# Kernel tuning notes

Hardware: AMD Instinct MI355X
Metric: run time of the kernel (lower is better)

The kernel has to match this reference:

```python
import jax, jax.numpy as jnp
import numpy as np

VOCAB, H, E, B, S = 50257, 1024, 1024, 64, 2048


def setup_inputs() -> dict:
    key = jax.random.key(0)
    ks = jax.random.split(key, 12)
    s = 0.02
    return {
        "input_seq": jax.random.randint(ks[0], (B,), 0, VOCAB),
        "last_hidden": jax.random.normal(ks[1], (1, B, H), jnp.float32),
        "last_cell": jax.random.normal(ks[2], (1, B, H), jnp.float32),
        "encoder_outputs": jax.random.normal(ks[3], (S, B, H), jnp.float32),
        "emb_W": jax.random.normal(ks[4], (VOCAB, E), jnp.float32) * s,
        "W_ih": jax.random.normal(ks[5], (4 * H, E), jnp.float32) * s,
        "W_hh": jax.random.normal(ks[6], (4 * H, H), jnp.float32) * s,
        "b_ih": jnp.zeros((4 * H,), jnp.float32),
        "b_hh": jnp.zeros((4 * H,), jnp.float32),
        "concat_W": jax.random.normal(ks[7], (H, 2 * H), jnp.float32) * s,
        "concat_b": jnp.zeros((H,), jnp.float32),
        "out_W": jax.random.normal(ks[8], (VOCAB, H), jnp.float32) * s,
        "out_b": jnp.zeros((VOCAB,), jnp.float32),
    }


def reference(input_seq, last_hidden, last_cell, encoder_outputs,
              emb_W, W_ih, W_hh, b_ih, b_hh,
              concat_W, concat_b, out_W, out_b):
    # Embedding lookup (dropout is identity in eval mode)
    x = emb_W[input_seq]                      # [B, E]
    h0 = last_hidden[0]                       # [B, H]
    c0 = last_cell[0]                         # [B, H]
    # Single LSTM step (PyTorch gate order: i, f, g, o)
    gates = x @ W_ih.T + b_ih + h0 @ W_hh.T + b_hh   # [B, 4H]
    i, f, g, o = jnp.split(gates, 4, axis=-1)
    c = jax.nn.sigmoid(f) * c0 + jax.nn.sigmoid(i) * jnp.tanh(g)
    h = jax.nn.sigmoid(o) * jnp.tanh(c)       # [B, H] == rnn_output
    # 'dot' attention: energies[b, s] = h[b] . enc[s, b]  (vectorized)
    energies = jnp.einsum('bh,sbh->bs', h, encoder_outputs)   # [B, S]
    attn = jax.nn.softmax(energies, axis=1)                   # [B, S]
    context = jnp.einsum('bs,sbh->bh', attn, encoder_outputs) # [B, H]
    concat_out = jnp.tanh(jnp.concatenate([h, context], axis=1) @ concat_W.T + concat_b)
    output = concat_out @ out_W.T + out_b                     # [B, VOCAB]
    return output, h[None], c[None], attn[:, None, :]
```

## Files before the change

### kernel.cpp

```cpp
#include <hip/hip_runtime.h>
#include <hip/hip_bf16.h>
#include <math.h>

#define BB 64
#define HH 1024
#define SS 2048
#define VV 50257

typedef float f32x4 __attribute__((ext_vector_type(4)));
typedef short bf16x8 __attribute__((ext_vector_type(8)));

__device__ __forceinline__ float sigf(float x){ return 1.0f/(1.0f+__expf(-x)); }
__device__ __forceinline__ short f2bf(float f){
  __hip_bfloat16 h = __float2bfloat16(f);
  return __builtin_bit_cast(short, h);
}

__global__ void k_embed(const int* __restrict__ seq, const float* __restrict__ embW,
                        float* __restrict__ x){
  int b = blockIdx.x;
  int k = threadIdx.x * 4;
  const float4 v = *reinterpret_cast<const float4*>(embW + (size_t)seq[b]*HH + k);
  *reinterpret_cast<float4*>(x + (size_t)b*HH + k) = v;
}

__global__ __launch_bounds__(256)
void k_gemm(const float* __restrict__ A1, const float* __restrict__ W1,
            const float* __restrict__ A2, const float* __restrict__ W2,
            float* __restrict__ dst, int N, int K, int ldw)
{
  __shared__ float As[64][33];
  __shared__ float Ws[128][33];
  const int tid = threadIdx.x;
  const int nb = blockIdx.x, sk = blockIdx.y, SK = gridDim.y;
  const int ntiles = 2 * (K >> 5);
  const int tps = ntiles / SK;
  const int t0 = sk * tps;
  const int bg = tid & 15, ng = tid >> 4;

  float acc[4][8];
  #pragma unroll
  for (int i = 0; i < 4; ++i)
    #pragma unroll
    for (int j = 0; j < 8; ++j) acc[i][j] = 0.f;

  const int ar = tid >> 2, ac = (tid & 3) * 8;
  const int wr = tid >> 1, wc = (tid & 1) * 16;
  const int wn = nb * 128 + wr;

  for (int t = t0; t < t0 + tps; ++t) {
    const int kt = t << 5;
    const float* A; const float* W; int kk;
    if (kt < K) { A = A1; W = W1; kk = kt; } else { A = A2; W = W2; kk = kt - K; }
    {
      const float* s = A + (size_t)ar * K + kk + ac;
      float4 v0 = *(const float4*)s;
      float4 v1 = *(const float4*)(s + 4);
      As[ar][ac+0]=v0.x; As[ar][ac+1]=v0.y; As[ar][ac+2]=v0.z; As[ar][ac+3]=v0.w;
      As[ar][ac+4]=v1.x; As[ar][ac+5]=v1.y; As[ar][ac+6]=v1.z; As[ar][ac+7]=v1.w;
    }
    if (wn < N) {
      const float* s = W + (size_t)wn * ldw + kk + wc;
      float4 v0 = *(const float4*)s;
      float4 v1 = *(const float4*)(s + 4);
      float4 v2 = *(const float4*)(s + 8);
      float4 v3 = *(const float4*)(s + 12);
      Ws[wr][wc+0]=v0.x;  Ws[wr][wc+1]=v0.y;  Ws[wr][wc+2]=v0.z;  Ws[wr][wc+3]=v0.w;
      Ws[wr][wc+4]=v1.x;  Ws[wr][wc+5]=v1.y;  Ws[wr][wc+6]=v1.z;  Ws[wr][wc+7]=v1.w;
      Ws[wr][wc+8]=v2.x;  Ws[wr][wc+9]=v2.y;  Ws[wr][wc+10]=v2.z; Ws[wr][wc+11]=v2.w;
      Ws[wr][wc+12]=v3.x; Ws[wr][wc+13]=v3.y; Ws[wr][wc+14]=v3.z; Ws[wr][wc+15]=v3.w;
    }
    __syncthreads();
    #pragma unroll 8
    for (int k = 0; k < 32; ++k) {
      const float a0 = As[bg*4+0][k], a1 = As[bg*4+1][k];
      const float a2 = As[bg*4+2][k], a3 = As[bg*4+3][k];
      #pragma unroll
      for (int j = 0; j < 8; ++j) {
        const float w = Ws[ng*8+j][k];
        acc[0][j] += a0*w; acc[1][j] += a1*w; acc[2][j] += a2*w; acc[3][j] += a3*w;
      }
    }
    __syncthreads();
  }

  #pragma unroll
  for (int j = 0; j < 8; ++j) {
    const int n = nb*128 + ng*8 + j;
    if (n < N)
      #pragma unroll
      for (int i = 0; i < 4; ++i)
        dst[((size_t)sk*64 + (bg*4+i))*N + n] = acc[i][j];
  }
}

__global__ __launch_bounds__(256)
void k_mfma(const short* __restrict__ A, int lda,
            const float* __restrict__ W1, const float* __restrict__ W2,
            int K1, int ldw, const float* __restrict__ bias,
            float* __restrict__ dst, short* __restrict__ dstb,
            int N, int Ktot, int direct, int act)
{
  const int tid  = threadIdx.x;
  const int wave = tid >> 6, lane = tid & 63;
  const int nb = blockIdx.x, sk = blockIdx.y, SK = gridDim.y;
  const int ksteps = Ktot >> 5;
  const int kps = ksteps / SK;
  const int k0 = sk * kps;
  const int n0 = nb*128 + wave*32;
  const int r = lane & 15, g = lane >> 4;

  f32x4 acc[4][2] = {};

  for (int ks = k0; ks < k0 + kps; ++ks) {
    const int kk = (ks << 5) + g*8;
    bf16x8 af[4];
    #pragma unroll
    for (int mf = 0; mf < 4; ++mf)
      af[mf] = *(const bf16x8*)(A + (size_t)(mf*16 + r)*lda + kk);
    #pragma unroll
    for (int nf = 0; nf < 2; ++nf) {
      const int n = n0 + nf*16 + r;
      bf16x8 bfr = {};
      if (n < N) {
        const float* wp = (kk < K1) ? (W1 + (size_t)n*ldw + kk)
                                    : (W2 + (size_t)n*ldw + (kk - K1));
        float4 w0 = *(const float4*)wp;
        float4 w1 = *(const float4*)(wp + 4);
        bfr[0]=f2bf(w0.x); bfr[1]=f2bf(w0.y); bfr[2]=f2bf(w0.z); bfr[3]=f2bf(w0.w);
        bfr[4]=f2bf(w1.x); bfr[5]=f2bf(w1.y); bfr[6]=f2bf(w1.z); bfr[7]=f2bf(w1.w);
      }
      #pragma unroll
      for (int mf = 0; mf < 4; ++mf)
        acc[mf][nf] = __builtin_amdgcn_mfma_f32_16x16x32_bf16(af[mf], bfr, acc[mf][nf], 0, 0, 0);
    }
  }

  if (direct) {
    #pragma unroll
    for (int nf = 0; nf < 2; ++nf) {
      const int n = n0 + nf*16 + r;
      if (n < N) {
        const float bv = bias ? bias[n] : 0.f;
        #pragma unroll
        for (int mf = 0; mf < 4; ++mf)
          #pragma unroll
          for (int j = 0; j < 4; ++j) {
            float v = acc[mf][nf][j] + bv;
            if (act == 1) v = tanhf(v);
            const int row = mf*16 + g*4 + j;
            if (dst)  dst[(size_t)row*N + n] = v;
            if (dstb) dstb[(size_t)row*N + n] = f2bf(v);
          }
      }
    }
  } else {
    #pragma unroll
    for (int nf = 0; nf < 2; ++nf) {
      const int n = n0 + nf*16 + r;
      if (n < N)
        #pragma unroll
        for (int mf = 0; mf < 4; ++mf)
          #pragma unroll
          for (int j = 0; j < 4; ++j)
            dst[((size_t)sk*64 + (mf*16 + g*4 + j))*N + n] = acc[mf][nf][j];
    }
  }
}

__global__ void k_reduce(const float* __restrict__ part, const float* __restrict__ bias1,
                         const float* __restrict__ bias2, float* __restrict__ dst,
                         short* __restrict__ dstb, int N, int SK, int act){
  size_t idx = (size_t)blockIdx.x*256 + threadIdx.x;
  if (idx >= (size_t)64*N) return;
  int b = (int)(idx / N), n = (int)(idx % N);
  float v = (bias1 ? bias1[n] : 0.f) + (bias2 ? bias2[n] : 0.f);
  for (int s = 0; s < SK; ++s) v += part[((size_t)s*64 + b)*N + n];
  if (act == 1) v = tanhf(v);
  if (dst)  dst[(size_t)b*N + n] = v;
  if (dstb) dstb[(size_t)b*N + n] = f2bf(v);
}

__global__ void k_lstm(const float* __restrict__ gates, const float* __restrict__ c0,
                       float* __restrict__ h_out, float* __restrict__ c_out,
                       short* __restrict__ concA){
  int idx = blockIdx.x*256 + threadIdx.x;
  int b = idx >> 10, k = idx & 1023;
  const float* g = gates + (size_t)b*4096;
  float gi = g[k], gf = g[1024+k], gg = g[2048+k], go = g[3072+k];
  float c = sigf(gf)*c0[idx] + sigf(gi)*tanhf(gg);
  float h = sigf(go)*tanhf(c);
  c_out[idx] = c;
  h_out[idx] = h;
  concA[(size_t)b*2048 + k] = f2bf(h);
}

__global__ __launch_bounds__(256)
void k_attn_part(const float* __restrict__ h, const float* __restrict__ enc,
                 float* __restrict__ energ, float* __restrict__ mpart,
                 float* __restrict__ lpart, float* __restrict__ ctxpart, int C){
  const int b  = blockIdx.x & 63;
  const int ch = blockIdx.x >> 6;
  const int wave = threadIdx.x >> 6;
  const int lane = threadIdx.x & 63;
  const int rows = SS / C;
  const int s0 = ch * rows;

  float4 hv0, hv1, hv2, hv3;
  {
    const float* hb = h + (size_t)b*HH + lane*16;
    hv0 = *(const float4*)(hb);   hv1 = *(const float4*)(hb+4);
    hv2 = *(const float4*)(hb+8); hv3 = *(const float4*)(hb+12);
  }
  float m = -INFINITY, l = 0.f;
  float cacc[16];
  #pragma unroll
  for (int j = 0; j < 16; ++j) cacc[j] = 0.f;

  for (int s = s0 + wave; s < s0 + rows; s += 4) {
    const float* ep = enc + ((size_t)s*BB + b)*HH + lane*16;
    const float4 e0 = *(const float4*)(ep);
    const float4 e1 = *(const float4*)(ep+4);
    const float4 e2 = *(const float4*)(ep+8);
    const float4 e3 = *(const float4*)(ep+12);
    float p = hv0.x*e0.x + hv0.y*e0.y + hv0.z*e0.z + hv0.w*e0.w
            + hv1.x*e1.x + hv1.y*e1.y + hv1.z*e1.z + hv1.w*e1.w
            + hv2.x*e2.x + hv2.y*e2.y + hv2.z*e2.z + hv2.w*e2.w
            + hv3.x*e3.x + hv3.y*e3.y + hv3.z*e3.z + hv3.w*e3.w;
    p += __shfl_xor(p, 1);  p += __shfl_xor(p, 2);  p += __shfl_xor(p, 4);
    p += __shfl_xor(p, 8);  p += __shfl_xor(p, 16); p += __shfl_xor(p, 32);
    if (lane == 0) energ[(size_t)b*SS + s] = p;
    const float mn = fmaxf(m, p);
    const float sc = __expf(m - mn);
    const float pe = __expf(p - mn);
    l = l*sc + pe;
    cacc[0]=cacc[0]*sc+pe*e0.x;  cacc[1]=cacc[1]*sc+pe*e0.y;
    cacc[2]=cacc[2]*sc+pe*e0.z;  cacc[3]=cacc[3]*sc+pe*e0.w;
    cacc[4]=cacc[4]*sc+pe*e1.x;  cacc[5]=cacc[5]*sc+pe*e1.y;
    cacc[6]=cacc[6]*sc+pe*e1.z;  cacc[7]=cacc[7]*sc+pe*e1.w;
    cacc[8]=cacc[8]*sc+pe*e2.x;  cacc[9]=cacc[9]*sc+pe*e2.y;
    cacc[10]=cacc[10]*sc+pe*e2.z; cacc[11]=cacc[11]*sc+pe*e2.w;
    cacc[12]=cacc[12]*sc+pe*e3.x; cacc[13]=cacc[13]*sc+pe*e3.y;
    cacc[14]=cacc[14]*sc+pe*e3.z; cacc[15]=cacc[15]*sc+pe*e3.w;
    m = mn;
  }

  __shared__ float sm[4], sl[4];
  __shared__ float sctx[4][1024];
  if (lane == 0) { sm[wave] = m; sl[wave] = l; }
  __syncthreads();
  const float mg = fmaxf(fmaxf(sm[0], sm[1]), fmaxf(sm[2], sm[3]));
  const float lg = sl[0]*__expf(sm[0]-mg) + sl[1]*__expf(sm[1]-mg)
                 + sl[2]*__expf(sm[2]-mg) + sl[3]*__expf(sm[3]-mg);
  const float scw = __expf(m - mg);
  #pragma unroll
  for (int j = 0; j < 16; ++j) sctx[wave][lane*16 + j] = cacc[j]*scw;
  __syncthreads();
  const int d = threadIdx.x * 4;
  const float4 a0 = *(const float4*)&sctx[0][d];
  const float4 a1 = *(const float4*)&sctx[1][d];
  const float4 a2 = *(const float4*)&sctx[2][d];
  const float4 a3 = *(const float4*)&sctx[3][d];
  float4 rr;
  rr.x = a0.x+a1.x+a2.x+a3.x; rr.y = a0.y+a1.y+a2.y+a3.y;
  rr.z = a0.z+a1.z+a2.z+a3.z; rr.w = a0.w+a1.w+a2.w+a3.w;
  *(float4*)(ctxpart + ((size_t)(b*C + ch))*HH + d) = rr;
  if (threadIdx.x == 0) { mpart[b*C+ch] = mg; lpart[b*C+ch] = lg; }
}

__global__ void k_attn_fin(const float* __restrict__ mpart, const float* __restrict__ lpart,
                           const float* __restrict__ ctxpart, const float* __restrict__ energ,
                           float* __restrict__ ctx, float* __restrict__ attn,
                           short* __restrict__ concA, int C){
  const int b = blockIdx.x, tid = threadIdx.x;
  float m = -INFINITY;
  for (int c = 0; c < C; ++c) m = fmaxf(m, mpart[b*C+c]);
  float l = 0.f;
  for (int c = 0; c < C; ++c) l += lpart[b*C+c] * __expf(mpart[b*C+c] - m);
  const float inv = 1.0f / l;
  float ax = 0.f, ay = 0.f, az = 0.f, aw = 0.f;
  for (int c = 0; c < C; ++c) {
    const float w = __expf(mpart[b*C+c] - m);
    const float* cp = ctxpart + ((size_t)(b*C+c))*HH + tid*4;
    ax += w*cp[0]; ay += w*cp[1]; az += w*cp[2]; aw += w*cp[3];
  }
  ax *= inv; ay *= inv; az *= inv; aw *= inv;
  float* o = ctx + (size_t)b*HH + tid*4;
  o[0] = ax; o[1] = ay; o[2] = az; o[3] = aw;
  short* ca = concA + (size_t)b*2048 + 1024 + tid*4;
  ca[0] = f2bf(ax); ca[1] = f2bf(ay); ca[2] = f2bf(az); ca[3] = f2bf(aw);
  for (int j = 0; j < 8; ++j) {
    const int s = j*256 + tid;
    attn[(size_t)b*SS + s] = __expf(energ[(size_t)b*SS + s] - m) * inv;
  }
}

extern "C" void kernel_launch(void* const* d_in, const int* in_sizes, int n_in,
                              void* d_out, int out_size, void* d_ws, size_t ws_size,
                              hipStream_t stream){
  const int*   seq  = (const int*)  d_in[0];
  const float* h0   = (const float*)d_in[1];
  const float* c0   = (const float*)d_in[2];
  const float* enc  = (const float*)d_in[3];
  const float* embW = (const float*)d_in[4];
  const float* W_ih = (const float*)d_in[5];
  const float* W_hh = (const float*)d_in[6];
  const float* b_ih = (const float*)d_in[7];
  const float* b_hh = (const float*)d_in[8];
  const float* cW   = (const float*)d_in[9];
  const float* cb   = (const float*)d_in[10];
  const float* oW   = (const float*)d_in[11];
  const float* ob   = (const float*)d_in[12];
  float* out = (float*)d_out;

  float* ws = (float*)d_ws;
  const size_t o_x = 0, o_gates = 65536, o_energ = 327680, o_ctx = 458752,
               o_concA = 524288, o_concB = 589824, o_dyn = 622592;
  const size_t SKPART = 4194304;
  int C = 32;
  for (;;) {
    size_t need = (o_dyn + (size_t)C*128 + (size_t)C*65536 + SKPART) * sizeof(float);
    if (need <= ws_size || C == 1) break;
    C >>= 1;
  }
  float* x       = ws + o_x;
  float* gates   = ws + o_gates;
  float* energ   = ws + o_energ;
  float* ctx     = ws + o_ctx;
  short* concA   = (short*)(ws + o_concA);
  short* concB   = (short*)(ws + o_concB);
  float* mpart   = ws + o_dyn;
  float* lpart   = mpart + (size_t)64*C;
  float* ctxpart = lpart + (size_t)64*C;
  float* skpart  = ctxpart + (size_t)64*C*1024;

  const size_t o_h = 3216448, o_c = 3281984, o_attn = 3347520;

  k_embed<<<64, 256, 0, stream>>>(seq, embW, x);

  k_gemm<<<dim3(32,16), 256, 0, stream>>>(x, W_ih, h0, W_hh, skpart, 4096, 1024, 1024);
  k_reduce<<<1024, 256, 0, stream>>>(skpart, b_ih, b_hh, gates, nullptr, 4096, 16, 0);

  k_lstm<<<256, 256, 0, stream>>>(gates, c0, out + o_h, out + o_c, concA);

  k_attn_part<<<64*C, 256, 0, stream>>>(out + o_h, enc, energ, mpart, lpart, ctxpart, C);
  k_attn_fin<<<64, 256, 0, stream>>>(mpart, lpart, ctxpart, energ, ctx,
                                     out + o_attn, concA, C);

  k_mfma<<<dim3(8,32), 256, 0, stream>>>(concA, 2048, cW, nullptr, 2048, 2048,
                                         nullptr, skpart, nullptr, 1024, 2048, 0, 0);
  k_reduce<<<256, 256, 0, stream>>>(skpart, cb, nullptr, nullptr, concB, 1024, 32, 1);

  k_mfma<<<dim3(393,1), 256, 0, stream>>>(concB, 1024, oW, nullptr, 1024, 1024,
                                          ob, out, nullptr, 50257, 1024, 1, 0);
}
```

Before: 271.6 us.

## Fuse embedding gather, bias-reduce and LSTM; pipeline logits GEMM loads

Folds the embedding gather into the gates GEMM by indexing emb_W rows directly. It merges the split-K reduction with the LSTM cell update, so two launches and the gates round trip disappear. A dedicated logits kernel software-pipelines its fp32 weight loads one k-step ahead, and the attention partial kernel processes two sequence rows per iteration. It also halves the split-K factor for the concat GEMM and drops the unused ctx store. The pipelined logits kernel uses more registers, and the smaller split-K reduces parallelism for the concat GEMM.

```diff
diff --git a/kernel.cpp b/kernel.cpp
--- a/kernel.cpp
+++ b/kernel.cpp
@@ -16,25 +16,17 @@
   return __builtin_bit_cast(short, h);
 }
 
-__global__ void k_embed(const int* __restrict__ seq, const float* __restrict__ embW,
-                        float* __restrict__ x){
-  int b = blockIdx.x;
-  int k = threadIdx.x * 4;
-  const float4 v = *reinterpret_cast<const float4*>(embW + (size_t)seq[b]*HH + k);
-  *reinterpret_cast<float4*>(x + (size_t)b*HH + k) = v;
-}
-
 __global__ __launch_bounds__(256)
-void k_gemm(const float* __restrict__ A1, const float* __restrict__ W1,
-            const float* __restrict__ A2, const float* __restrict__ W2,
-            float* __restrict__ dst, int N, int K, int ldw)
+void k_gates(const int* __restrict__ seq, const float* __restrict__ embW,
+             const float* __restrict__ h0,
+             const float* __restrict__ W_ih, const float* __restrict__ W_hh,
+             float* __restrict__ dst)
 {
   __shared__ float As[64][33];
   __shared__ float Ws[128][33];
   const int tid = threadIdx.x;
   const int nb = blockIdx.x, sk = blockIdx.y, SK = gridDim.y;
-  const int ntiles = 2 * (K >> 5);
-  const int tps = ntiles / SK;
+  const int tps = 64 / SK;
   const int t0 = sk * tps;
   const int bg = tid & 15, ng = tid >> 4;
 
@@ -47,20 +39,27 @@
   const int ar = tid >> 2, ac = (tid & 3) * 8;
   const int wr = tid >> 1, wc = (tid & 1) * 16;
   const int wn = nb * 128 + wr;
+  const int erow = seq[ar];
 
   for (int t = t0; t < t0 + tps; ++t) {
     const int kt = t << 5;
-    const float* A; const float* W; int kk;
-    if (kt < K) { A = A1; W = W1; kk = kt; } else { A = A2; W = W2; kk = kt - K; }
+    const float* abase; const float* wbase;
+    if (kt < 1024) {
+      abase = embW + (size_t)erow*1024 + kt;
+      wbase = W_ih + (size_t)wn*1024 + kt;
+    } else {
+      abase = h0 + (size_t)ar*1024 + (kt - 1024);
+      wbase = W_hh + (size_t)wn*1024 + (kt - 1024);
+    }
     {
-      const float* s = A + (size_t)ar * K + kk + ac;
+      const float* s = abase + ac;
       float4 v0 = *(const float4*)s;
       float4 v1 = *(const float4*)(s + 4);
       As[ar][ac+0]=v0.x; As[ar][ac+1]=v0.y; As[ar][ac+2]=v0.z; As[ar][ac+3]=v0.w;
       As[ar][ac+4]=v1.x; As[ar][ac+5]=v1.y; As[ar][ac+6]=v1.z; As[ar][ac+7]=v1.w;
     }
-    if (wn < N) {
-      const float* s = W + (size_t)wn * ldw + kk + wc;
+    {
+      const float* s = wbase + wc;
       float4 v0 = *(const float4*)s;
       float4 v1 = *(const float4*)(s + 4);
       float4 v2 = *(const float4*)(s + 8);
@@ -87,19 +86,38 @@
   #pragma unroll
   for (int j = 0; j < 8; ++j) {
     const int n = nb*128 + ng*8 + j;
-    if (n < N)
-      #pragma unroll
-      for (int i = 0; i < 4; ++i)
-        dst[((size_t)sk*64 + (bg*4+i))*N + n] = acc[i][j];
-  }
+    #pragma unroll
+    for (int i = 0; i < 4; ++i)
+      dst[((size_t)sk*64 + (bg*4+i))*4096 + n] = acc[i][j];
+  }
+}
+
+__global__ void k_rlstm(const float* __restrict__ part, const float* __restrict__ b_ih,
+                        const float* __restrict__ b_hh, const float* __restrict__ c0,
+                        float* __restrict__ h_out, float* __restrict__ c_out,
+                        short* __restrict__ concA, int SK){
+  int idx = blockIdx.x*256 + threadIdx.x;
+  int b = idx >> 10, k = idx & 1023;
+  float gi = b_ih[k]      + b_hh[k];
+  float gf = b_ih[1024+k] + b_hh[1024+k];
+  float gg = b_ih[2048+k] + b_hh[2048+k];
+  float go = b_ih[3072+k] + b_hh[3072+k];
+  const float* p = part + (size_t)b*4096 + k;
+  for (int s = 0; s < SK; ++s) {
+    const float* ps = p + (size_t)s*64*4096;
+    gi += ps[0]; gf += ps[1024]; gg += ps[2048]; go += ps[3072];
+  }
+  float c = sigf(gf)*c0[idx] + sigf(gi)*tanhf(gg);
+  float h = sigf(go)*tanhf(c);
+  c_out[idx] = c;
+  h_out[idx] = h;
+  concA[(size_t)b*2048 + k] = f2bf(h);
 }
 
 __global__ __launch_bounds__(256)
 void k_mfma(const short* __restrict__ A, int lda,
-            const float* __restrict__ W1, const float* __restrict__ W2,
-            int K1, int ldw, const float* __restrict__ bias,
-            float* __restrict__ dst, short* __restrict__ dstb,
-            int N, int Ktot, int direct, int act)
+            const float* __restrict__ W1, int ldw,
+            float* __restrict__ dst, int N, int Ktot)
 {
   const int tid  = threadIdx.x;
   const int wave = tid >> 6, lane = tid & 63;
@@ -121,78 +139,105 @@
     #pragma unroll
     for (int nf = 0; nf < 2; ++nf) {
       const int n = n0 + nf*16 + r;
-      bf16x8 bfr = {};
-      if (n < N) {
-        const float* wp = (kk < K1) ? (W1 + (size_t)n*ldw + kk)
-                                    : (W2 + (size_t)n*ldw + (kk - K1));
-        float4 w0 = *(const float4*)wp;
-        float4 w1 = *(const float4*)(wp + 4);
-        bfr[0]=f2bf(w0.x); bfr[1]=f2bf(w0.y); bfr[2]=f2bf(w0.z); bfr[3]=f2bf(w0.w);
-        bfr[4]=f2bf(w1.x); bfr[5]=f2bf(w1.y); bfr[6]=f2bf(w1.z); bfr[7]=f2bf(w1.w);
-      }
+      const float* wp = W1 + (size_t)n*ldw + kk;
+      float4 w0 = *(const float4*)wp;
+      float4 w1 = *(const float4*)(wp + 4);
+      bf16x8 bfr;
+      bfr[0]=f2bf(w0.x); bfr[1]=f2bf(w0.y); bfr[2]=f2bf(w0.z); bfr[3]=f2bf(w0.w);
+      bfr[4]=f2bf(w1.x); bfr[5]=f2bf(w1.y); bfr[6]=f2bf(w1.z); bfr[7]=f2bf(w1.w);
       #pragma unroll
       for (int mf = 0; mf < 4; ++mf)
         acc[mf][nf] = __builtin_amdgcn_mfma_f32_16x16x32_bf16(af[mf], bfr, acc[mf][nf], 0, 0, 0);
     }
   }
 
-  if (direct) {
+  #pragma unroll
+  for (int nf = 0; nf < 2; ++nf) {
+    const int n = n0 + nf*16 + r;
     #pragma unroll
-    for (int nf = 0; nf < 2; ++nf) {
-      const int n = n0 + nf*16 + r;
-      if (n < N) {
-        const float bv = bias ? bias[n] : 0.f;
-        #pragma unroll
-        for (int mf = 0; mf < 4; ++mf)
-          #pragma unroll
-          for (int j = 0; j < 4; ++j) {
-            float v = acc[mf][nf][j] + bv;
-            if (act == 1) v = tanhf(v);
-            const int row = mf*16 + g*4 + j;
-            if (dst)  dst[(size_t)row*N + n] = v;
-            if (dstb) dstb[(size_t)row*N + n] = f2bf(v);
-          }
-      }
-    }
-  } else {
-    #pragma unroll
-    for (int nf = 0; nf < 2; ++nf) {
-      const int n = n0 + nf*16 + r;
-      if (n < N)
-        #pragma unroll
-        for (int mf = 0; mf < 4; ++mf)
-          #pragma unroll
-          for (int j = 0; j < 4; ++j)
-            dst[((size_t)sk*64 + (mf*16 + g*4 + j))*N + n] = acc[mf][nf][j];
-    }
-  }
-}
-
-__global__ void k_reduce(const float* __restrict__ part, const float* __restrict__ bias1,
-                         const float* __restrict__ bias2, float* __restrict__ dst,
-                         short* __restrict__ dstb, int N, int SK, int act){
+    for (int mf = 0; mf < 4; ++mf)
+      #pragma unroll
+      for (int j = 0; j < 4; ++j)
+        dst[((size_t)sk*64 + (mf*16 + g*4 + j))*N + n] = acc[mf][nf][j];
+  }
+}
+
+__global__ void k_reduce(const float* __restrict__ part, const float* __restrict__ bias,
+                         short* __restrict__ dstb, int N, int SK){
   size_t idx = (size_t)blockIdx.x*256 + threadIdx.x;
   if (idx >= (size_t)64*N) return;
   int b = (int)(idx / N), n = (int)(idx % N);
-  float v = (bias1 ? bias1[n] : 0.f) + (bias2 ? bias2[n] : 0.f);
+  float v = bias[n];
   for (int s = 0; s < SK; ++s) v += part[((size_t)s*64 + b)*N + n];
-  if (act == 1) v = tanhf(v);
-  if (dst)  dst[(size_t)b*N + n] = v;
-  if (dstb) dstb[(size_t)b*N + n] = f2bf(v);
-}
-
-__global__ void k_lstm(const float* __restrict__ gates, const float* __restrict__ c0,
-                       float* __restrict__ h_out, float* __restrict__ c_out,
-                       short* __restrict__ concA){
-  int idx = blockIdx.x*256 + threadIdx.x;
-  int b = idx >> 10, k = idx & 1023;
-  const float* g = gates + (size_t)b*4096;
-  float gi = g[k], gf = g[1024+k], gg = g[2048+k], go = g[3072+k];
-  float c = sigf(gf)*c0[idx] + sigf(gi)*tanhf(gg);
-  float h = sigf(go)*tanhf(c);
-  c_out[idx] = c;
-  h_out[idx] = h;
-  concA[(size_t)b*2048 + k] = f2bf(h);
+  dstb[(size_t)b*N + n] = f2bf(tanhf(v));
+}
+
+__global__ __launch_bounds__(256)
+void k_logits(const short* __restrict__ A, const float* __restrict__ W,
+              const float* __restrict__ bias, float* __restrict__ out)
+{
+  const int tid = threadIdx.x;
+  const int wave = tid >> 6, lane = tid & 63;
+  const int r = lane & 15, g = lane >> 4;
+  const int n0 = blockIdx.x*128 + wave*32;
+  const int nA = n0 + r, nB = n0 + 16 + r;
+  const float* wA = W + (size_t)(nA < VV ? nA : 0)*1024;
+  const float* wB = W + (size_t)(nB < VV ? nB : 0)*1024;
+  const short* A0 = A + (size_t)r*1024 + g*8;
+
+  f32x4 acc[4][2] = {};
+
+  bf16x8 a0,a1,a2,a3; float4 u0,u1,v0,v1;
+  {
+    const int kk = g*8;
+    a0 = *(const bf16x8*)(A0);
+    a1 = *(const bf16x8*)(A0 + 16*1024);
+    a2 = *(const bf16x8*)(A0 + 32*1024);
+    a3 = *(const bf16x8*)(A0 + 48*1024);
+    u0 = *(const float4*)(wA + kk); u1 = *(const float4*)(wA + kk + 4);
+    v0 = *(const float4*)(wB + kk); v1 = *(const float4*)(wB + kk + 4);
+  }
+
+  #pragma unroll
+  for (int ks = 0; ks < 32; ++ks) {
+    bf16x8 ca0=a0, ca1=a1, ca2=a2, ca3=a3;
+    float4 cu0=u0, cu1=u1, cv0=v0, cv1=v1;
+    if (ks < 31) {
+      const int kk = (ks+1)*32 + g*8;
+      a0 = *(const bf16x8*)(A0 + (ks+1)*32);
+      a1 = *(const bf16x8*)(A0 + 16*1024 + (ks+1)*32);
+      a2 = *(const bf16x8*)(A0 + 32*1024 + (ks+1)*32);
+      a3 = *(const bf16x8*)(A0 + 48*1024 + (ks+1)*32);
+      u0 = *(const float4*)(wA + kk); u1 = *(const float4*)(wA + kk + 4);
+      v0 = *(const float4*)(wB + kk); v1 = *(const float4*)(wB + kk + 4);
+    }
+    bf16x8 bA, bB;
+    bA[0]=f2bf(cu0.x); bA[1]=f2bf(cu0.y); bA[2]=f2bf(cu0.z); bA[3]=f2bf(cu0.w);
+    bA[4]=f2bf(cu1.x); bA[5]=f2bf(cu1.y); bA[6]=f2bf(cu1.z); bA[7]=f2bf(cu1.w);
+    bB[0]=f2bf(cv0.x); bB[1]=f2bf(cv0.y); bB[2]=f2bf(cv0.z); bB[3]=f2bf(cv0.w);
+    bB[4]=f2bf(cv1.x); bB[5]=f2bf(cv1.y); bB[6]=f2bf(cv1.z); bB[7]=f2bf(cv1.w);
+    acc[0][0] = __builtin_amdgcn_mfma_f32_16x16x32_bf16(ca0, bA, acc[0][0], 0,0,0);
+    acc[1][0] = __builtin_amdgcn_mfma_f32_16x16x32_bf16(ca1, bA, acc[1][0], 0,0,0);
+    acc[2][0] = __builtin_amdgcn_mfma_f32_16x16x32_bf16(ca2, bA, acc[2][0], 0,0,0);
+    acc[3][0] = __builtin_amdgcn_mfma_f32_16x16x32_bf16(ca3, bA, acc[3][0], 0,0,0);
+    acc[0][1] = __builtin_amdgcn_mfma_f32_16x16x32_bf16(ca0, bB, acc[0][1], 0,0,0);
+    acc[1][1] = __builtin_amdgcn_mfma_f32_16x16x32_bf16(ca1, bB, acc[1][1], 0,0,0);
+    acc[2][1] = __builtin_amdgcn_mfma_f32_16x16x32_bf16(ca2, bB, acc[2][1], 0,0,0);
+    acc[3][1] = __builtin_amdgcn_mfma_f32_16x16x32_bf16(ca3, bB, acc[3][1], 0,0,0);
+  }
+
+  #pragma unroll
+  for (int nf = 0; nf < 2; ++nf) {
+    const int n = n0 + nf*16 + r;
+    if (n < VV) {
+      const float bv = bias[n];
+      #pragma unroll
+      for (int mf = 0; mf < 4; ++mf)
+        #pragma unroll
+        for (int j = 0; j < 4; ++j)
+          out[(size_t)(mf*16 + g*4 + j)*VV + n] = acc[mf][nf][j] + bv;
+    }
+  }
 }
 
 __global__ __launch_bounds__(256)
@@ -204,7 +249,8 @@
   const int wave = threadIdx.x >> 6;
   const int lane = threadIdx.x & 63;
   const int rows = SS / C;
-  const int s0 = ch * rows;
+  const int rpw  = rows >> 2;
+  const int sw = ch*rows + wave*rpw;
 
   float4 hv0, hv1, hv2, hv3;
   {
@@ -217,31 +263,56 @@
   #pragma unroll
   for (int j = 0; j < 16; ++j) cacc[j] = 0.f;
 
-  for (int s = s0 + wave; s < s0 + rows; s += 4) {
-    const float* ep = enc + ((size_t)s*BB + b)*HH + lane*16;
+  for (int i = 0; i < rpw; i += 2) {
+    const float* ep = enc + ((size_t)(sw+i)*BB + b)*HH + lane*16;
+    const float* fp = ep + (size_t)BB*HH;
     const float4 e0 = *(const float4*)(ep);
     const float4 e1 = *(const float4*)(ep+4);
     const float4 e2 = *(const float4*)(ep+8);
     const float4 e3 = *(const float4*)(ep+12);
+    const float4 f0 = *(const float4*)(fp);
+    const float4 f1 = *(const float4*)(fp+4);
+    const float4 f2 = *(const float4*)(fp+8);
+    const float4 f3 = *(const float4*)(fp+12);
     float p = hv0.x*e0.x + hv0.y*e0.y + hv0.z*e0.z + hv0.w*e0.w
             + hv1.x*e1.x + hv1.y*e1.y + hv1.z*e1.z + hv1.w*e1.w
             + hv2.x*e2.x + hv2.y*e2.y + hv2.z*e2.z + hv2.w*e2.w
             + hv3.x*e3.x + hv3.y*e3.y + hv3.z*e3.z + hv3.w*e3.w;
-    p += __shfl_xor(p, 1);  p += __shfl_xor(p, 2);  p += __shfl_xor(p, 4);
-    p += __shfl_xor(p, 8);  p += __shfl_xor(p, 16); p += __shfl_xor(p, 32);
-    if (lane == 0) energ[(size_t)b*SS + s] = p;
-    const float mn = fmaxf(m, p);
+    float q = hv0.x*f0.x + hv0.y*f0.y + hv0.z*f0.z + hv0.w*f0.w
+            + hv1.x*f1.x + hv1.y*f1.y + hv1.z*f1.z + hv1.w*f1.w
+            + hv2.x*f2.x + hv2.y*f2.y + hv2.z*f2.z + hv2.w*f2.w
+            + hv3.x*f3.x + hv3.y*f3.y + hv3.z*f3.z + hv3.w*f3.w;
+    p += __shfl_xor(p, 1);  q += __shfl_xor(q, 1);
+    p += __shfl_xor(p, 2);  q += __shfl_xor(q, 2);
+    p += __shfl_xor(p, 4);  q += __shfl_xor(q, 4);
+    p += __shfl_xor(p, 8);  q += __shfl_xor(q, 8);
+    p += __shfl_xor(p, 16); q += __shfl_xor(q, 16);
+    p += __shfl_xor(p, 32); q += __shfl_xor(q, 32);
+    if (lane == 0) {
+      float2 pq; pq.x = p; pq.y = q;
+      *(float2*)(energ + (size_t)b*SS + sw + i) = pq;
+    }
+    const float mn = fmaxf(fmaxf(m, p), q);
     const float sc = __expf(m - mn);
     const float pe = __expf(p - mn);
-    l = l*sc + pe;
-    cacc[0]=cacc[0]*sc+pe*e0.x;  cacc[1]=cacc[1]*sc+pe*e0.y;
-    cacc[2]=cacc[2]*sc+pe*e0.z;  cacc[3]=cacc[3]*sc+pe*e0.w;
-    cacc[4]=cacc[4]*sc+pe*e1.x;  cacc[5]=cacc[5]*sc+pe*e1.y;
-    cacc[6]=cacc[6]*sc+pe*e1.z;  cacc[7]=cacc[7]*sc+pe*e1.w;
-    cacc[8]=cacc[8]*sc+pe*e2.x;  cacc[9]=cacc[9]*sc+pe*e2.y;
-    cacc[10]=cacc[10]*sc+pe*e2.z; cacc[11]=cacc[11]*sc+pe*e2.w;
-    cacc[12]=cacc[12]*sc+pe*e3.x; cacc[13]=cacc[13]*sc+pe*e3.y;
-    cacc[14]=cacc[14]*sc+pe*e3.z; cacc[15]=cacc[15]*sc+pe*e3.w;
+    const float qe = __expf(q - mn);
+    l = l*sc + pe + qe;
+    cacc[0] = cacc[0]*sc + pe*e0.x + qe*f0.x;
+    cacc[1] = cacc[1]*sc + pe*e0.y + qe*f0.y;
+    cacc[2] = cacc[2]*sc + pe*e0.z + qe*f0.z;
+    cacc[3] = cacc[3]*sc + pe*e0.w + qe*f0.w;
+    cacc[4] = cacc[4]*sc + pe*e1.x + qe*f1.x;
+    cacc[5] = cacc[5]*sc + pe*e1.y + qe*f1.y;
+    cacc[6] = cacc[6]*sc + pe*e1.z + qe*f1.z;
+    cacc[7] = cacc[7]*sc + pe*e1.w + qe*f1.w;
+    cacc[8] = cacc[8]*sc + pe*e2.x + qe*f2.x;
+    cacc[9] = cacc[9]*sc + pe*e2.y + qe*f2.y;
+    cacc[10] = cacc[10]*sc + pe*e2.z + qe*f2.z;
+    cacc[11] = cacc[11]*sc + pe*e2.w + qe*f2.w;
+    cacc[12] = cacc[12]*sc + pe*e3.x + qe*f3.x;
+    cacc[13] = cacc[13]*sc + pe*e3.y + qe*f3.y;
+    cacc[14] = cacc[14]*sc + pe*e3.z + qe*f3.z;
+    cacc[15] = cacc[15]*sc + pe*e3.w + qe*f3.w;
     m = mn;
   }
 
@@ -270,8 +341,7 @@
 
 __global__ void k_attn_fin(const float* __restrict__ mpart, const float* __restrict__ lpart,
                            const float* __restrict__ ctxpart, const float* __restrict__ energ,
-                           float* __restrict__ ctx, float* __restrict__ attn,
-                           short* __restrict__ concA, int C){
+                           float* __restrict__ attn, short* __restrict__ concA, int C){
   const int b = blockIdx.x, tid = threadIdx.x;
   float m = -INFINITY;
   for (int c = 0; c < C; ++c) m = fmaxf(m, mpart[b*C+c]);
@@ -285,8 +355,6 @@
     ax += w*cp[0]; ay += w*cp[1]; az += w*cp[2]; aw += w*cp[3];
   }
   ax *= inv; ay *= inv; az *= inv; aw *= inv;
-  float* o = ctx + (size_t)b*HH + tid*4;
-  o[0] = ax; o[1] = ay; o[2] = az; o[3] = aw;
   short* ca = concA + (size_t)b*2048 + 1024 + tid*4;
   ca[0] = f2bf(ax); ca[1] = f2bf(ay); ca[2] = f2bf(az); ca[3] = f2bf(aw);
   for (int j = 0; j < 8; ++j) {
@@ -314,43 +382,33 @@
   float* out = (float*)d_out;
 
   float* ws = (float*)d_ws;
-  const size_t o_x = 0, o_gates = 65536, o_energ = 327680, o_ctx = 458752,
-               o_concA = 524288, o_concB = 589824, o_dyn = 622592;
-  const size_t SKPART = 4194304;
+  const size_t o_energ = 0;
+  const size_t o_concA = 131072;
+  const size_t o_concB = 196608;
+  const size_t o_mp    = 229376;
+  const size_t SKPART  = 4194304;
   int C = 32;
   for (;;) {
-    size_t need = (o_dyn + (size_t)C*128 + (size_t)C*65536 + SKPART) * sizeof(float);
+    size_t need = (o_mp + (size_t)64*C*2 + (size_t)64*C*1024 + SKPART) * sizeof(float);
     if (need <= ws_size || C == 1) break;
     C >>= 1;
   }
-  float* x       = ws + o_x;
-  float* gates   = ws + o_gates;
   float* energ   = ws + o_energ;
-  float* ctx     = ws + o_ctx;
   short* concA   = (short*)(ws + o_concA);
   short* concB   = (short*)(ws + o_concB);
-  float* mpart   = ws + o_dyn;
+  float* mpart   = ws + o_mp;
   float* lpart   = mpart + (size_t)64*C;
   float* ctxpart = lpart + (size_t)64*C;
   float* skpart  = ctxpart + (size_t)64*C*1024;
 
   const size_t o_h = 3216448, o_c = 3281984, o_attn = 3347520;
 
-  k_embed<<<64, 256, 0, stream>>>(seq, embW, x);
-
-  k_gemm<<<dim3(32,16), 256, 0, stream>>>(x, W_ih, h0, W_hh, skpart, 4096, 1024, 1024);
-  k_reduce<<<1024, 256, 0, stream>>>(skpart, b_ih, b_hh, gates, nullptr, 4096, 16, 0);
-
-  k_lstm<<<256, 256, 0, stream>>>(gates, c0, out + o_h, out + o_c, concA);
-
+  k_gates<<<dim3(32,16), 256, 0, stream>>>(seq, embW, h0, W_ih, W_hh, skpart);
+  k_rlstm<<<256, 256, 0, stream>>>(skpart, b_ih, b_hh, c0, out + o_h, out + o_c,
+                                   concA, 16);
   k_attn_part<<<64*C, 256, 0, stream>>>(out + o_h, enc, energ, mpart, lpart, ctxpart, C);
-  k_attn_fin<<<64, 256, 0, stream>>>(mpart, lpart, ctxpart, energ, ctx,
-                                     out + o_attn, concA, C);
-
-  k_mfma<<<dim3(8,32), 256, 0, stream>>>(concA, 2048, cW, nullptr, 2048, 2048,
-                                         nullptr, skpart, nullptr, 1024, 2048, 0, 0);
-  k_reduce<<<256, 256, 0, stream>>>(skpart, cb, nullptr, nullptr, concB, 1024, 32, 1);
-
-  k_mfma<<<dim3(393,1), 256, 0, stream>>>(concB, 1024, oW, nullptr, 1024, 1024,
-                                          ob, out, nullptr, 50257, 1024, 1, 0);
-}
+  k_attn_fin<<<64, 256, 0, stream>>>(mpart, lpart, ctxpart, energ, out + o_attn, concA, C);
+  k_mfma<<<dim3(8,16), 256, 0, stream>>>(concA, 2048, cW, 2048, skpart, 1024, 2048);
+  k_reduce<<<256, 256, 0, stream>>>(skpart, cb, concB, 1024, 16);
+  k_logits<<<393, 256, 0, stream>>>(concB, oW, ob, out);
+}
```

New measurement: 267.4 us. No clear change (-1.6%).
